# Performance work log

Measured on AMD Instinct MI355X. Metric: run time of the kernel, lower is better.

The kernel has to match this reference:

```python
import jax, jax.numpy as jnp
import numpy as np

B, T, D, KQ, K, V, L = 4, 4096, 256, 32, 4, 8, 4
LN_EPS = 1e-5


def _layernorm(h, g, b):
    mu = h.mean(-1, keepdims=True)
    var = ((h - mu) ** 2).mean(-1, keepdims=True)
    return (h - mu) * jax.lax.rsqrt(var + LN_EPS) * g + b


def _forward(x, attention_mask, Wq, bq, Wk, bk, Wg, bg, W1f, b1f, W2f, b2f,
             ln_g, ln_b, Whh, b_ih, b_hh, Wp, bp, opW1, opb1, opW2, opb2, Wo, bo):
    # ---- DemandRouter ----
    q = x @ Wq + bq                      # [B,T,KQ]
    k = x @ Wk + bk                      # [B,T,KQ]
    sim = jnp.einsum('btk,bsk->bts', q, k) / jnp.sqrt(jnp.float32(KQ))  # [B,T,T]
    mask2 = attention_mask[:, None, :] * attention_mask[:, :, None]
    sim = jnp.where(mask2 == 0, jnp.float32(-1e9), sim)
    gates = jax.nn.sigmoid(x @ Wg + bg)[..., 0]   # [B,T]
    sim = sim * gates[:, :, None]
    _, idx = jax.lax.top_k(sim, K)                # [B,T,K]
    gathered = jax.vmap(lambda xb, ib: xb[ib])(x, idx)  # [B,T,K,D]
    routed_mean = gathered.mean(axis=2)           # [B,T,D]
    # ---- System1Block ----
    ffn = jax.nn.gelu(routed_mean @ W1f + b1f, approximate=False) @ W2f + b2f
    h = _layernorm(routed_mean + ffn, ln_g, ln_b)  # [B,T,D]
    # ---- ProgramGenerator (GRU over zero inputs, h0 = mean-pooled context) ----
    hs = h.mean(axis=1)                           # [B,D]
    outs = []
    for _ in range(L):
        gh = hs @ Whh.T + b_hh                    # [B,3D]
        r = jax.nn.sigmoid(b_ih[:D] + gh[:, :D])
        z = jax.nn.sigmoid(b_ih[D:2 * D] + gh[:, D:2 * D])
        n = jnp.tanh(b_ih[2 * D:] + r * gh[:, 2 * D:])
        hs = (1 - z) * n + z * hs
        outs.append(hs)
    rnn_out = jnp.stack(outs, axis=1)             # [B,L,D]
    program_logits = rnn_out @ Wp + bp            # [B,L,V]
    # ---- NeuralOpLibrary: op outputs are identical across L, so compute once
    # on [B,T,D] and average softmax weights over L (same math as expand+mean).
    op_hidden = jax.nn.relu(jnp.einsum('btd,vde->btve', h, opW1) + opb1)
    op_out = jnp.einsum('btve,ved->btvd', op_hidden, opW2) + opb2  # [B,T,V,D]
    w = jax.nn.softmax(program_logits, axis=-1).mean(axis=1)       # [B,V]
    fused = jnp.einsum('bv,btvd->btd', w, op_out)                   # [B,T,D]
    # ---- pool + output projection ----
    pooled = fused.max(axis=1)                    # [B,D]
    return pooled @ Wo + bo


def setup_inputs() -> dict:
    key = jax.random.key(0)
    ks = jax.random.split(key, 20)
    s = 0.02
    p = lambda i, shape: jax.random.normal(ks[i], shape, jnp.float32) * s
    return {
        'x': jax.random.normal(ks[0], (B, T, D), jnp.float32),
        'attention_mask': jnp.ones((B, T), jnp.float32),
        'Wq': p(1, (D, KQ)), 'bq': jnp.zeros((KQ,), jnp.float32),
        'Wk': p(2, (D, KQ)), 'bk': jnp.zeros((KQ,), jnp.float32),
        'Wg': p(3, (D, 1)), 'bg': jnp.zeros((1,), jnp.float32),
        'W1f': p(4, (D, 2 * D)), 'b1f': jnp.zeros((2 * D,), jnp.float32),
        'W2f': p(5, (2 * D, D)), 'b2f': jnp.zeros((D,), jnp.float32),
        'ln_g': jnp.ones((D,), jnp.float32), 'ln_b': jnp.zeros((D,), jnp.float32),
        'Whh': p(6, (3 * D, D)), 'b_ih': p(7, (3 * D,)), 'b_hh': p(8, (3 * D,)),
        'Wp': p(9, (D, V)), 'bp': jnp.zeros((V,), jnp.float32),
        'opW1': p(10, (V, D, D)), 'opb1': jnp.zeros((V, D), jnp.float32),
        'opW2': p(11, (V, D, D)), 'opb2': jnp.zeros((V, D), jnp.float32),
        'Wo': p(12, (D, D)), 'bo': jnp.zeros((D,), jnp.float32),
    }


def reference(x, attention_mask, Wq, bq, Wk, bk, Wg, bg, W1f, b1f, W2f, b2f,
              ln_g, ln_b, Whh, b_ih, b_hh, Wp, bp, opW1, opb1, opW2, opb2, Wo, bo):
    return _forward(x, attention_mask, Wq, bq, Wk, bk, Wg, bg, W1f, b1f, W2f, b2f,
                    ln_g, ln_b, Whh, b_ih, b_hh, Wp, bp, opW1, opb1, opW2, opb2, Wo, bo)
```

## Files before the change

### kernel.cpp

```cpp
#include <hip/hip_runtime.h>

#define BB 4
#define TT 4096
#define DD 256
#define KQ 32
#define TOPK 4
#define NV 8
#define NL 4
#define MROWS (BB*TT)
#define NSC 8
#define SSPAN 512
#define NCAND (NSC*16)

typedef __attribute__((ext_vector_type(8))) __bf16 bf16x8;
typedef __attribute__((ext_vector_type(4))) float  f32x4;

__device__ __forceinline__ unsigned short f2bf(float f) {
  union { float f; unsigned u; } un; un.f = f;
  unsigned r = un.u + 0x7fffu + ((un.u >> 16) & 1u);
  return (unsigned short)(r >> 16);
}
__device__ __forceinline__ float b2f(unsigned short s) {
  union { unsigned u; float f; } un; un.u = ((unsigned)s) << 16;
  return un.f;
}

__device__ __forceinline__ void ins4(float val, int s, float v[4], int id[4]) {
  if (val <= v[3]) return;
  v[3] = val; id[3] = s;
  #pragma unroll
  for (int j = 3; j > 0; --j) {
    if (v[j] > v[j-1]) {
      float tv = v[j]; v[j] = v[j-1]; v[j-1] = tv;
      int   ti = id[j]; id[j] = id[j-1]; id[j-1] = ti;
    }
  }
}

__global__ __launch_bounds__(256) void prep_weights(
    const float* __restrict__ W1f, const float* __restrict__ W2f,
    const float* __restrict__ opW1, const float* __restrict__ opW2,
    const float* __restrict__ Whh,
    unsigned short* __restrict__ W1ft, unsigned short* __restrict__ W2ft,
    unsigned short* __restrict__ opW1t, unsigned short* __restrict__ opW2t,
    unsigned int* __restrict__ Whhp) {
  int idx = blockIdx.x * 256 + threadIdx.x;
  if (idx < 131072) { int n = idx >> 8, d = idx & 255; W1ft[idx] = f2bf(W1f[d*512 + n]); return; }
  idx -= 131072;
  if (idx < 131072) { int n = idx >> 9, d = idx & 511; W2ft[idx] = f2bf(W2f[d*256 + n]); return; }
  idx -= 131072;
  if (idx < 524288) { int np = idx >> 8, d = idx & 255; int v = np >> 8, e = np & 255;
                      opW1t[idx] = f2bf(opW1[v*65536 + d*256 + e]); return; }
  idx -= 524288;
  if (idx < 524288) { int n = idx >> 11, kp = idx & 2047; int v = kp >> 8, k2 = kp & 255;
                      opW2t[idx] = f2bf(opW2[v*65536 + k2*256 + n]); return; }
  idx -= 524288;
  if (idx < 98304) {
    int dp = idx / 768, j = idx - dp*768;
    unsigned lo = f2bf(Whh[j*256 + 2*dp]);
    unsigned hi = f2bf(Whh[j*256 + 2*dp + 1]);
    Whhp[idx] = lo | (hi << 16);
  }
}

__global__ __launch_bounds__(256) void qk_proj(
    const float* __restrict__ x, const float* __restrict__ Wq, const float* __restrict__ bq,
    const float* __restrict__ Wk, const float* __restrict__ bk,
    float* __restrict__ q, float* __restrict__ kk,
    unsigned short* __restrict__ qbf, unsigned short* __restrict__ kbf) {
  __shared__ float xs[1024];
  int tid = threadIdx.x;
  *(float4*)&xs[tid*4] = *(const float4*)&x[(size_t)blockIdx.x*1024 + tid*4];
  __syncthreads();
  int row = blockIdx.x*4 + (tid >> 6);
  int j = tid & 63;
  int jj = j & 31;
  const float* W = (j < 32) ? Wq : Wk;
  const float* xr = &xs[(tid >> 6) * 256];
  float acc = 0.f;
  #pragma unroll 8
  for (int d = 0; d < 256; ++d) acc += xr[d] * W[d*32 + jj];
  acc += (j < 32) ? bq[jj] : bk[jj];
  float* out = (j < 32) ? q : kk;
  unsigned short* outb = (j < 32) ? qbf : kbf;
  out[(size_t)row*32 + jj] = acc;
  outb[(size_t)row*32 + jj] = f2bf(acc);
}

__global__ __launch_bounds__(256) void sim_scan(
    const unsigned short* __restrict__ qbf, const unsigned short* __restrict__ kbf,
    const float* __restrict__ mask, int* __restrict__ candi, float* __restrict__ candvv) {
  int b = blockIdx.z, sc = blockIdx.y;
  int q0 = blockIdx.x * 64;
  int tid = threadIdx.x;
  int w = tid >> 6, lane = tid & 63;
  int l15 = lane & 15, lhi = lane >> 4;

  __shared__ unsigned short kfr[SSPAN*32];
  __shared__ float ms[SSPAN];
  __shared__ int mflag;

  int qrow = q0 + w*16 + l15;
  bf16x8 qf = *(const bf16x8*)&qbf[((size_t)b*TT + qrow)*32 + lhi*8];
  float mrow = mask[b*TT + qrow];

  float vtop[4]; int itop[4];
  #pragma unroll
  for (int r = 0; r < 4; ++r) { vtop[r] = -__builtin_inff(); itop[r] = 0; }

  int s0 = sc * SSPAN;
  if (tid == 0) mflag = 0;
  __syncthreads();
  int anyzero = 0;
  #pragma unroll
  for (int rr = 0; rr < 2; ++rr) {
    int s = rr*256 + tid;
    const unsigned short* src = &kbf[((size_t)b*TT + s0 + s)*32];
    uint4 d0 = *(const uint4*)(src);
    uint4 d1 = *(const uint4*)(src + 8);
    uint4 d2 = *(const uint4*)(src + 16);
    uint4 d3 = *(const uint4*)(src + 24);
    int fb = (s >> 4)*512 + (s & 15)*8;
    *(uint4*)&kfr[fb +   0] = d0;
    *(uint4*)&kfr[fb + 128] = d1;
    *(uint4*)&kfr[fb + 256] = d2;
    *(uint4*)&kfr[fb + 384] = d3;
    float mv = mask[b*TT + s0 + s];
    ms[s] = mv;
    if (mv == 0.f) anyzero = 1;
  }
  if (anyzero) mflag = 1;
  __syncthreads();
  bool useMask = (mflag != 0) || (mrow == 0.f);
  f32x4 z = {0.f, 0.f, 0.f, 0.f};
  for (int sf = 0; sf < SSPAN/16; sf += 2) {
    bf16x8 a0 = *(const bf16x8*)&kfr[(sf+0)*512 + lane*8];
    bf16x8 a1 = *(const bf16x8*)&kfr[(sf+1)*512 + lane*8];
    f32x4 c0 = __builtin_amdgcn_mfma_f32_16x16x32_bf16(a0, qf, z, 0, 0, 0);
    f32x4 c1 = __builtin_amdgcn_mfma_f32_16x16x32_bf16(a1, qf, z, 0, 0, 0);
    int sb0 = s0 + (sf+0)*16 + lhi*4;
    int sb1 = s0 + (sf+1)*16 + lhi*4;
    #pragma unroll
    for (int r = 0; r < 4; ++r) {
      float v0 = c0[r], v1 = c1[r];
      if (useMask) {
        if (mrow * ms[(sf+0)*16 + lhi*4 + r] == 0.f) v0 = -1e9f;
        if (mrow * ms[(sf+1)*16 + lhi*4 + r] == 0.f) v1 = -1e9f;
      }
      ins4(v0, sb0 + r, vtop, itop);
      ins4(v1, sb1 + r, vtop, itop);
    }
  }
  size_t base = ((size_t)(b*TT + qrow))*NCAND + sc*16 + lhi*4;
  #pragma unroll
  for (int r = 0; r < 4; ++r) { candi[base + r] = itop[r]; candvv[base + r] = vtop[r]; }
}

__global__ __launch_bounds__(256) void refine8(
    const int* __restrict__ candi, const float* __restrict__ candv,
    const float* __restrict__ q, const float* __restrict__ kk,
    const float* __restrict__ mask, int* __restrict__ sel) {
  int tid = threadIdx.x;
  int g = tid >> 5, j = tid & 31;
  int row = blockIdx.x*8 + g;
  int b = row >> 12;
  float v[4]; int id[4];
  const float* cvp = &candv[(size_t)row*NCAND];
  const int*   cip = &candi[(size_t)row*NCAND];
  #pragma unroll
  for (int k2 = 0; k2 < 4; ++k2) { v[k2] = cvp[j + k2*32]; id[k2] = cip[j + k2*32]; }
  int c8[8];
  #pragma unroll
  for (int r = 0; r < 8; ++r) {
    float bv = v[0]; int bi = id[0];
    #pragma unroll
    for (int k2 = 1; k2 < 4; ++k2)
      if (v[k2] > bv || (v[k2] == bv && id[k2] < bi)) { bv = v[k2]; bi = id[k2]; }
    #pragma unroll
    for (int o = 16; o > 0; o >>= 1) {
      float ov = __shfl_xor(bv, o, 32);
      int   oi = __shfl_xor(bi, o, 32);
      if (ov > bv || (ov == bv && oi < bi)) { bv = ov; bi = oi; }
    }
    c8[r] = bi;
    #pragma unroll
    for (int k2 = 0; k2 < 4; ++k2) if (id[k2] == bi) v[k2] = -__builtin_inff();
  }
  int ca = c8[j >> 2];
  int seg = (j & 3) * 8;
  const float* kp = &kk[((size_t)(b << 12) + ca)*32 + seg];
  const float* qp = &q[(size_t)row*32 + seg];
  float pd = 0.f;
  #pragma unroll
  for (int t = 0; t < 8; t += 4) {
    float4 kv = *(const float4*)&kp[t];
    float4 qv = *(const float4*)&qp[t];
    pd += kv.x*qv.x + kv.y*qv.y + kv.z*qv.z + kv.w*qv.w;
  }
  pd += __shfl_xor(pd, 1, 32);
  pd += __shfl_xor(pd, 2, 32);
  if (mask[row] * mask[(b << 12) + ca] == 0.f) pd = -1e9f;
  float dv[8];
  #pragma unroll
  for (int c = 0; c < 8; ++c) dv[c] = __shfl(pd, c*4, 32);
  if (j == 0) {
    int s0 = -1, s1 = -1, s2 = -1, s3 = -1;
    int4 o4;
    #pragma unroll
    for (int r = 0; r < 4; ++r) {
      float bv = -__builtin_inff(); int bi = 0x7fffffff;
      #pragma unroll
      for (int c = 0; c < 8; ++c) {
        int ii = c8[c]; float vv = dv[c];
        if (ii == s0 || ii == s1 || ii == s2 || ii == s3) continue;
        if (vv > bv || (vv == bv && ii < bi)) { bv = vv; bi = ii; }
      }
      if (r == 0) { o4.x = bi; s0 = bi; }
      else if (r == 1) { o4.y = bi; s1 = bi; }
      else if (r == 2) { o4.z = bi; s2 = bi; }
      else { o4.w = bi; s3 = bi; }
    }
    *(int4*)&sel[(size_t)row*4] = o4;
  }
}

__global__ __launch_bounds__(256) void gather_mean(
    const int* __restrict__ sel, const float* __restrict__ x,
    unsigned short* __restrict__ rmb) {
  int tid = threadIdx.x;
  int row = blockIdx.x*4 + (tid >> 6);
  int lane = tid & 63;
  int b = row >> 12;
  int4 s = *(const int4*)&sel[(size_t)row*4];
  const float* xb = &x[(size_t)b*TT*DD];
  float4 a  = *(const float4*)&xb[(size_t)s.x*DD + lane*4];
  float4 bb = *(const float4*)&xb[(size_t)s.y*DD + lane*4];
  float4 cc = *(const float4*)&xb[(size_t)s.z*DD + lane*4];
  float4 e  = *(const float4*)&xb[(size_t)s.w*DD + lane*4];
  ushort4 o;
  o.x = f2bf((a.x + bb.x + cc.x + e.x)*0.25f);
  o.y = f2bf((a.y + bb.y + cc.y + e.y)*0.25f);
  o.z = f2bf((a.z + bb.z + cc.z + e.z)*0.25f);
  o.w = f2bf((a.w + bb.w + cc.w + e.w)*0.25f);
  *(ushort4*)&rmb[(size_t)row*DD + lane*4] = o;
}

template<int EPI>
__global__ __launch_bounds__(256) void gemm_bf16(
    const unsigned short* __restrict__ A, const unsigned short* __restrict__ Bt,
    int Ndim, int Kdim,
    const float* __restrict__ bias,
    const unsigned short* __restrict__ resB,
    const float* __restrict__ auxf,
    float* __restrict__ outF, unsigned short* __restrict__ outB) {
  __shared__ unsigned short As[128*64];
  __shared__ unsigned short Bs[128*64];
  int tid = threadIdx.x;
  int lane = tid & 63, wid = tid >> 6;
  int wm = wid >> 1, wn = wid & 1;
  int l16 = lane & 15, lhi = lane >> 4;
  int m0 = blockIdx.x * 128, n0 = blockIdx.y * 128;
  f32x4 acc[4][4] = {};
  for (int kt = 0; kt < Kdim; kt += 64) {
    __syncthreads();
    #pragma unroll
    for (int i = 0; i < 4; ++i) {
      int L = i*256 + tid;
      int r = L >> 3, c = L & 7;
      int cs = c ^ (r & 7);
      uint4 va = *(const uint4*)(A  + (size_t)(m0 + r)*Kdim + kt + c*8);
      *(uint4*)&As[r*64 + cs*8] = va;
      uint4 vb = *(const uint4*)(Bt + (size_t)(n0 + r)*Kdim + kt + c*8);
      *(uint4*)&Bs[r*64 + cs*8] = vb;
    }
    __syncthreads();
    #pragma unroll
    for (int ks = 0; ks < 2; ++ks) {
      bf16x8 af[4], bfr[4];
      int kc = ks*4 + lhi;
      #pragma unroll
      for (int f = 0; f < 4; ++f) {
        int ra = wm*64 + f*16 + l16;
        af[f]  = *(const bf16x8*)&As[ra*64 + ((kc ^ (ra & 7)))*8];
        int rb = wn*64 + f*16 + l16;
        bfr[f] = *(const bf16x8*)&Bs[rb*64 + ((kc ^ (rb & 7)))*8];
      }
      #pragma unroll
      for (int mf = 0; mf < 4; ++mf)
        #pragma unroll
        for (int nf = 0; nf < 4; ++nf)
          acc[mf][nf] = __builtin_amdgcn_mfma_f32_16x16x32_bf16(af[mf], bfr[nf], acc[mf][nf], 0, 0, 0);
    }
  }
  #pragma unroll
  for (int mf = 0; mf < 4; ++mf) {
    #pragma unroll
    for (int nf = 0; nf < 4; ++nf) {
      #pragma unroll
      for (int r = 0; r < 4; ++r) {
        int row = m0 + wm*64 + mf*16 + lhi*4 + r;
        int col = n0 + wn*64 + nf*16 + l16;
        float v = acc[mf][nf][r];
        if constexpr (EPI == 0) {
          v += bias[col];
          v = 0.5f * v * (1.0f + erff(v * 0.70710678118654752f));
          outB[(size_t)row*Ndim + col] = f2bf(v);
        } else if constexpr (EPI == 1) {
          v += bias[col] + b2f(resB[(size_t)row*Ndim + col]);
          outF[(size_t)row*Ndim + col] = v;
        } else if constexpr (EPI == 2) {
          v += bias[col];
          v = fmaxf(v, 0.0f) * auxf[(row >> 12)*8 + (col >> 8)];
          outB[(size_t)row*Ndim + col] = f2bf(v);
        } else {
          v += auxf[(row >> 12)*256 + col];
          outB[(size_t)row*Ndim + col] = f2bf(v);
        }
      }
    }
  }
}

__global__ __launch_bounds__(256) void gemm64_bf16(
    const unsigned short* __restrict__ A, const unsigned short* __restrict__ Bt,
    int Ndim, int Kdim,
    const float* __restrict__ auxf, unsigned short* __restrict__ outB) {
  __shared__ unsigned short As[64*64];
  __shared__ unsigned short Bs[128*64];
  int tid = threadIdx.x;
  int lane = tid & 63, wn = tid >> 6;
  int l16 = lane & 15, lhi = lane >> 4;
  int m0 = blockIdx.x * 64, n0 = blockIdx.y * 128;
  f32x4 acc[4][2] = {};
  for (int kt = 0; kt < Kdim; kt += 64) {
    __syncthreads();
    #pragma unroll
    for (int i = 0; i < 2; ++i) {
      int L = i*256 + tid;
      int r = L >> 3, c = L & 7;
      int cs = c ^ (r & 7);
      uint4 va = *(const uint4*)(A + (size_t)(m0 + r)*Kdim + kt + c*8);
      *(uint4*)&As[r*64 + cs*8] = va;
    }
    #pragma unroll
    for (int i = 0; i < 4; ++i) {
      int L = i*256 + tid;
      int r = L >> 3, c = L & 7;
      int cs = c ^ (r & 7);
      uint4 vb = *(const uint4*)(Bt + (size_t)(n0 + r)*Kdim + kt + c*8);
      *(uint4*)&Bs[r*64 + cs*8] = vb;
    }
    __syncthreads();
    #pragma unroll
    for (int ks = 0; ks < 2; ++ks) {
      bf16x8 af[4], bfr[2];
      int kc = ks*4 + lhi;
      #pragma unroll
      for (int f = 0; f < 4; ++f) {
        int ra = f*16 + l16;
        af[f] = *(const bf16x8*)&As[ra*64 + ((kc ^ (ra & 7)))*8];
      }
      #pragma unroll
      for (int f = 0; f < 2; ++f) {
        int rb = wn*32 + f*16 + l16;
        bfr[f] = *(const bf16x8*)&Bs[rb*64 + ((kc ^ (rb & 7)))*8];
      }
      #pragma unroll
      for (int mf = 0; mf < 4; ++mf)
        #pragma unroll
        for (int nf = 0; nf < 2; ++nf)
          acc[mf][nf] = __builtin_amdgcn_mfma_f32_16x16x32_bf16(af[mf], bfr[nf], acc[mf][nf], 0, 0, 0);
    }
  }
  #pragma unroll
  for (int mf = 0; mf < 4; ++mf) {
    #pragma unroll
    for (int nf = 0; nf < 2; ++nf) {
      #pragma unroll
      for (int r = 0; r < 4; ++r) {
        int row = m0 + mf*16 + lhi*4 + r;
        int col = n0 + wn*32 + nf*16 + l16;
        float v = acc[mf][nf][r] + auxf[(row >> 12)*256 + col];
        outB[(size_t)row*Ndim + col] = f2bf(v);
      }
    }
  }
}

__global__ __launch_bounds__(256) void ln_kernel(
    const float* __restrict__ preLN, const float* __restrict__ g,
    const float* __restrict__ bta, unsigned short* __restrict__ h) {
  int tid = threadIdx.x;
  int lane = tid & 63;
  int row = blockIdx.x*4 + (tid >> 6);
  float4 v = *(const float4*)&preLN[(size_t)row*256 + lane*4];
  float s = v.x + v.y + v.z + v.w;
  #pragma unroll
  for (int o = 32; o > 0; o >>= 1) s += __shfl_xor(s, o);
  float mu = s * (1.0f/256.0f);
  float4 d; d.x = v.x-mu; d.y = v.y-mu; d.z = v.z-mu; d.w = v.w-mu;
  float s2 = d.x*d.x + d.y*d.y + d.z*d.z + d.w*d.w;
  #pragma unroll
  for (int o = 32; o > 0; o >>= 1) s2 += __shfl_xor(s2, o);
  float rstd = rsqrtf(s2 * (1.0f/256.0f) + 1e-5f);
  float4 gv = *(const float4*)&g[lane*4];
  float4 bv = *(const float4*)&bta[lane*4];
  ushort4 o;
  o.x = f2bf(d.x*rstd*gv.x + bv.x);
  o.y = f2bf(d.y*rstd*gv.y + bv.y);
  o.z = f2bf(d.z*rstd*gv.z + bv.z);
  o.w = f2bf(d.w*rstd*gv.w + bv.w);
  *(ushort4*)&h[(size_t)row*256 + lane*4] = o;
}

__global__ __launch_bounds__(256) void hsum_kernel(const unsigned short* __restrict__ h, float* __restrict__ hpart) {
  int c = blockIdx.x, b = blockIdx.y, d = threadIdx.x;
  const unsigned short* hp = &h[((size_t)(b*TT + c*64))*256 + d];
  float s = 0.f;
  #pragma unroll 8
  for (int i = 0; i < 64; ++i) s += b2f(hp[i*256]);
  hpart[(b*64 + c)*256 + d] = s;
}

__global__ __launch_bounds__(256) void gru_kernel(
    const float* __restrict__ hpart, const unsigned int* __restrict__ Whhp,
    const float* __restrict__ b_ih, const float* __restrict__ b_hh,
    const float* __restrict__ Wp, const float* __restrict__ bp,
    const float* __restrict__ opb2, float* __restrict__ w, float* __restrict__ wb2) {
  int b = blockIdx.x, tid = threadIdx.x;
  __shared__ float hs[256];
  __shared__ float wps[2048];
  __shared__ float lgpart[256];
  __shared__ float lg[8];
  __shared__ float wacc[8];
  float s = 0.f;
  for (int c = 0; c < 64; ++c) s += hpart[(b*64 + c)*256 + tid];
  hs[tid] = s * (1.0f/4096.0f);
  #pragma unroll
  for (int i = 0; i < 8; ++i) wps[i*256 + tid] = Wp[i*256 + tid];
  if (tid < 8) wacc[tid] = 0.f;
  __syncthreads();
  for (int l = 0; l < NL; ++l) {
    float g0 = 0.f, g1 = 0.f, g2 = 0.f;
    #pragma unroll 16
    for (int dp = 0; dp < 128; ++dp) {
      float h0 = hs[2*dp], h1 = hs[2*dp + 1];
      unsigned w0 = Whhp[dp*768 + tid];
      unsigned w1 = Whhp[dp*768 + 256 + tid];
      unsigned w2 = Whhp[dp*768 + 512 + tid];
      g0 += b2f((unsigned short)(w0 & 0xffff))*h0 + b2f((unsigned short)(w0 >> 16))*h1;
      g1 += b2f((unsigned short)(w1 & 0xffff))*h0 + b2f((unsigned short)(w1 >> 16))*h1;
      g2 += b2f((unsigned short)(w2 & 0xffff))*h0 + b2f((unsigned short)(w2 >> 16))*h1;
    }
    g0 += b_hh[tid]; g1 += b_hh[256 + tid]; g2 += b_hh[512 + tid];
    float r = 1.f / (1.f + expf(-(b_ih[tid] + g0)));
    float z = 1.f / (1.f + expf(-(b_ih[256 + tid] + g1)));
    float n = tanhf(b_ih[512 + tid] + r * g2);
    float hnew = (1.f - z) * n + z * hs[tid];
    __syncthreads();
    hs[tid] = hnew;
    __syncthreads();
    {
      int dp2 = tid >> 3;
      float acc = 0.f;
      #pragma unroll
      for (int k2 = 0; k2 < 8; ++k2) acc += hs[dp2 + 32*k2] * wps[tid + 256*k2];
      lgpart[tid] = acc;
    }
    __syncthreads();
    if (tid < 8) {
      float acc = bp[tid];
      #pragma unroll
      for (int j = 0; j < 32; ++j) acc += lgpart[j*8 + tid];
      lg[tid] = acc;
    }
    __syncthreads();
    if (tid == 0) {
      float mx = lg[0];
      #pragma unroll
      for (int i = 1; i < 8; ++i) mx = fmaxf(mx, lg[i]);
      float sm = 0.f; float e[8];
      #pragma unroll
      for (int i = 0; i < 8; ++i) { e[i] = expf(lg[i] - mx); sm += e[i]; }
      #pragma unroll
      for (int i = 0; i < 8; ++i) wacc[i] += e[i] / sm;
    }
    __syncthreads();
  }
  if (tid < 8) w[b*8 + tid] = wacc[tid] * 0.25f;
  float acc = 0.f;
  #pragma unroll
  for (int v = 0; v < 8; ++v) acc += (wacc[v] * 0.25f) * opb2[v*256 + tid];
  wb2[b*256 + tid] = acc;
}

__global__ __launch_bounds__(256) void maxpool_kernel(const unsigned short* __restrict__ fusedB, float* __restrict__ mpart) {
  int c = blockIdx.x, b = blockIdx.y, d = threadIdx.x;
  const unsigned short* fp = &fusedB[((size_t)(b*TT + c*64))*256 + d];
  float m = -__builtin_inff();
  #pragma unroll 8
  for (int i = 0; i < 64; ++i) m = fmaxf(m, b2f(fp[i*256]));
  mpart[(b*64 + c)*256 + d] = m;
}

__global__ __launch_bounds__(256) void outproj_kernel(
    const float* __restrict__ mpart, const float* __restrict__ Wo,
    const float* __restrict__ bo, float* __restrict__ out) {
  int b = blockIdx.x, tid = threadIdx.x;
  __shared__ float pooled[256];
  float m = -__builtin_inff();
  for (int c = 0; c < 64; ++c) m = fmaxf(m, mpart[(b*64 + c)*256 + tid]);
  pooled[tid] = m;
  __syncthreads();
  float acc = bo[tid];
  for (int d = 0; d < 256; ++d) acc += pooled[d] * Wo[d*256 + tid];
  out[b*256 + tid] = acc;
}

extern "C" void kernel_launch(void* const* d_in, const int* in_sizes, int n_in,
                              void* d_out, int out_size, void* d_ws, size_t ws_size,
                              hipStream_t stream) {
  const float* x     = (const float*)d_in[0];
  const float* amask = (const float*)d_in[1];
  const float* Wq    = (const float*)d_in[2];
  const float* bq    = (const float*)d_in[3];
  const float* Wk    = (const float*)d_in[4];
  const float* bk    = (const float*)d_in[5];
  const float* W1f   = (const float*)d_in[8];
  const float* b1f   = (const float*)d_in[9];
  const float* W2f   = (const float*)d_in[10];
  const float* b2f   = (const float*)d_in[11];
  const float* ln_g  = (const float*)d_in[12];
  const float* ln_b  = (const float*)d_in[13];
  const float* Whh   = (const float*)d_in[14];
  const float* b_ih  = (const float*)d_in[15];
  const float* b_hh  = (const float*)d_in[16];
  const float* Wp    = (const float*)d_in[17];
  const float* bp    = (const float*)d_in[18];
  const float* opW1  = (const float*)d_in[19];
  const float* opb1  = (const float*)d_in[20];
  const float* opW2  = (const float*)d_in[21];
  const float* opb2  = (const float*)d_in[22];
  const float* Wo    = (const float*)d_in[23];
  const float* bo    = (const float*)d_in[24];
  (void)in_sizes; (void)n_in; (void)out_size; (void)ws_size;

  char* ws = (char*)d_ws;
  float*          q      = (float*)(ws + 0);
  float*          kk     = (float*)(ws + 2097152);
  unsigned short* qbf    = (unsigned short*)(ws + 4194304);
  unsigned short* kbf    = (unsigned short*)(ws + 5242880);
  int*            candi  = (int*)(ws + 6291456);
  float*          candv  = (float*)(ws + 14680064);
  unsigned short* rmb    = (unsigned short*)(ws + 23068672);
  unsigned short* G1     = (unsigned short*)(ws + 31457280);
  float*          preLN  = (float*)(ws + 48234496);
  unsigned short* G1all  = (unsigned short*)(ws + 0);
  unsigned short* h      = (unsigned short*)(ws + 67108864);
  unsigned short* W1ft   = (unsigned short*)(ws + 75497472);
  unsigned short* W2ft   = (unsigned short*)(ws + 75759616);
  unsigned short* opW1t  = (unsigned short*)(ws + 76021760);
  unsigned short* opW2t  = (unsigned short*)(ws + 77070336);
  unsigned int*   Whhp   = (unsigned int*)(ws + 78118912);
  float*          hpart  = (float*)(ws + 78512128);
  float*          wv     = (float*)(ws + 78774272);
  float*          wb2    = (float*)(ws + 78778368);
  float*          mpart  = (float*)(ws + 78782464);
  unsigned short* fusedB = (unsigned short*)(ws + 79044608);
  int*            sel    = (int*)(ws + 87433216);

  prep_weights<<<5504, 256, 0, stream>>>(W1f, W2f, opW1, opW2, Whh, W1ft, W2ft, opW1t, opW2t, Whhp);
  qk_proj<<<4096, 256, 0, stream>>>(x, Wq, bq, Wk, bk, q, kk, qbf, kbf);
  sim_scan<<<dim3(TT/64, NSC, BB), 256, 0, stream>>>(qbf, kbf, amask, candi, candv);
  refine8<<<MROWS/8, 256, 0, stream>>>(candi, candv, q, kk, amask, sel);
  gather_mean<<<MROWS/4, 256, 0, stream>>>(sel, x, rmb);
  gemm_bf16<0><<<dim3(128, 4), 256, 0, stream>>>(rmb, W1ft, 512, 256, b1f, nullptr, nullptr, nullptr, G1);
  gemm_bf16<1><<<dim3(128, 2), 256, 0, stream>>>(G1, W2ft, 256, 512, b2f, rmb, nullptr, preLN, nullptr);
  ln_kernel<<<4096, 256, 0, stream>>>(preLN, ln_g, ln_b, h);
  hsum_kernel<<<dim3(64, BB), 256, 0, stream>>>(h, hpart);
  gru_kernel<<<4, 256, 0, stream>>>(hpart, Whhp, b_ih, b_hh, Wp, bp, opb2, wv, wb2);
  gemm_bf16<2><<<dim3(128, 16), 256, 0, stream>>>(h, opW1t, 2048, 256, opb1, nullptr, wv, nullptr, G1all);
  gemm64_bf16<<<dim3(256, 2), 256, 0, stream>>>(G1all, opW2t, 256, 2048, wb2, fusedB);
  maxpool_kernel<<<dim3(64, BB), 256, 0, stream>>>(fusedB, mpart);
  outproj_kernel<<<4, 256, 0, stream>>>(mpart, Wo, bo, (float*)d_out);
}
```

Baseline: 301.7 us.

## Stage GEMM bf16 epilogues through LDS and vectorize GRU weight reads

```diff
diff --git a/kernel.cpp b/kernel.cpp
--- a/kernel.cpp
+++ b/kernel.cpp
@@ -43,7 +43,7 @@
     const float* __restrict__ Whh,
     unsigned short* __restrict__ W1ft, unsigned short* __restrict__ W2ft,
     unsigned short* __restrict__ opW1t, unsigned short* __restrict__ opW2t,
-    unsigned int* __restrict__ Whhp) {
+    unsigned int* __restrict__ Whhp2) {
   int idx = blockIdx.x * 256 + threadIdx.x;
   if (idx < 131072) { int n = idx >> 8, d = idx & 255; W1ft[idx] = f2bf(W1f[d*512 + n]); return; }
   idx -= 131072;
@@ -56,10 +56,10 @@
                       opW2t[idx] = f2bf(opW2[v*65536 + k2*256 + n]); return; }
   idx -= 524288;
   if (idx < 98304) {
-    int dp = idx / 768, j = idx - dp*768;
+    int j = idx >> 7, dp = idx & 127;
     unsigned lo = f2bf(Whh[j*256 + 2*dp]);
     unsigned hi = f2bf(Whh[j*256 + 2*dp + 1]);
-    Whhp[idx] = lo | (hi << 16);
+    Whhp2[idx] = lo | (hi << 16);
   }
 }
 
@@ -253,8 +253,9 @@
     const unsigned short* __restrict__ resB,
     const float* __restrict__ auxf,
     float* __restrict__ outF, unsigned short* __restrict__ outB) {
-  __shared__ unsigned short As[128*64];
-  __shared__ unsigned short Bs[128*64];
+  __shared__ unsigned short SMEM[128*132];
+  unsigned short* As = SMEM;
+  unsigned short* Bs = SMEM + 128*64;
   int tid = threadIdx.x;
   int lane = tid & 63, wid = tid >> 6;
   int wm = wid >> 1, wn = wid & 1;
@@ -292,31 +293,49 @@
           acc[mf][nf] = __builtin_amdgcn_mfma_f32_16x16x32_bf16(af[mf], bfr[nf], acc[mf][nf], 0, 0, 0);
     }
   }
-  #pragma unroll
-  for (int mf = 0; mf < 4; ++mf) {
-    #pragma unroll
-    for (int nf = 0; nf < 4; ++nf) {
-      #pragma unroll
-      for (int r = 0; r < 4; ++r) {
-        int row = m0 + wm*64 + mf*16 + lhi*4 + r;
-        int col = n0 + wn*64 + nf*16 + l16;
-        float v = acc[mf][nf][r];
-        if constexpr (EPI == 0) {
-          v += bias[col];
-          v = 0.5f * v * (1.0f + erff(v * 0.70710678118654752f));
-          outB[(size_t)row*Ndim + col] = f2bf(v);
-        } else if constexpr (EPI == 1) {
-          v += bias[col] + b2f(resB[(size_t)row*Ndim + col]);
+  if constexpr (EPI == 1) {
+    #pragma unroll
+    for (int mf = 0; mf < 4; ++mf)
+      #pragma unroll
+      for (int nf = 0; nf < 4; ++nf)
+        #pragma unroll
+        for (int r = 0; r < 4; ++r) {
+          int row = m0 + wm*64 + mf*16 + lhi*4 + r;
+          int col = n0 + wn*64 + nf*16 + l16;
+          float v = acc[mf][nf][r] + bias[col] + b2f(resB[(size_t)row*Ndim + col]);
           outF[(size_t)row*Ndim + col] = v;
-        } else if constexpr (EPI == 2) {
-          v += bias[col];
-          v = fmaxf(v, 0.0f) * auxf[(row >> 12)*8 + (col >> 8)];
-          outB[(size_t)row*Ndim + col] = f2bf(v);
-        } else {
-          v += auxf[(row >> 12)*256 + col];
-          outB[(size_t)row*Ndim + col] = f2bf(v);
         }
-      }
+  } else {
+    __syncthreads();
+    #pragma unroll
+    for (int mf = 0; mf < 4; ++mf) {
+      #pragma unroll
+      for (int nf = 0; nf < 4; ++nf) {
+        #pragma unroll
+        for (int r = 0; r < 4; ++r) {
+          int lrow = wm*64 + mf*16 + lhi*4 + r;
+          int lcol = wn*64 + nf*16 + l16;
+          int row = m0 + lrow, col = n0 + lcol;
+          float v = acc[mf][nf][r];
+          if constexpr (EPI == 0) {
+            v += bias[col];
+            v = 0.5f * v * (1.0f + erff(v * 0.70710678118654752f));
+          } else if constexpr (EPI == 2) {
+            v += bias[col];
+            v = fmaxf(v, 0.0f) * auxf[(row >> 12)*8 + (col >> 8)];
+          } else {
+            v += auxf[(row >> 12)*256 + col];
+          }
+          SMEM[lrow*132 + lcol] = f2bf(v);
+        }
+      }
+    }
+    __syncthreads();
+    #pragma unroll
+    for (int i = 0; i < 8; ++i) {
+      int idx = i*256 + tid;
+      int lrow = idx >> 4, co = (idx & 15)*8;
+      *(uint4*)&outB[(size_t)(m0 + lrow)*Ndim + n0 + co] = *(const uint4*)&SMEM[lrow*132 + co];
     }
   }
 }
@@ -325,8 +344,9 @@
     const unsigned short* __restrict__ A, const unsigned short* __restrict__ Bt,
     int Ndim, int Kdim,
     const float* __restrict__ auxf, unsigned short* __restrict__ outB) {
-  __shared__ unsigned short As[64*64];
-  __shared__ unsigned short Bs[128*64];
+  __shared__ unsigned short SMEM[64*192 + 64];
+  unsigned short* As = SMEM;
+  unsigned short* Bs = SMEM + 64*64;
   int tid = threadIdx.x;
   int lane = tid & 63, wn = tid >> 6;
   int l16 = lane & 15, lhi = lane >> 4;
@@ -372,18 +392,26 @@
           acc[mf][nf] = __builtin_amdgcn_mfma_f32_16x16x32_bf16(af[mf], bfr[nf], acc[mf][nf], 0, 0, 0);
     }
   }
+  __syncthreads();
   #pragma unroll
   for (int mf = 0; mf < 4; ++mf) {
     #pragma unroll
     for (int nf = 0; nf < 2; ++nf) {
       #pragma unroll
       for (int r = 0; r < 4; ++r) {
-        int row = m0 + mf*16 + lhi*4 + r;
-        int col = n0 + wn*32 + nf*16 + l16;
-        float v = acc[mf][nf][r] + auxf[(row >> 12)*256 + col];
-        outB[(size_t)row*Ndim + col] = f2bf(v);
-      }
-    }
+        int lrow = mf*16 + lhi*4 + r;
+        int lcol = wn*32 + nf*16 + l16;
+        float v = acc[mf][nf][r] + auxf[((m0 + lrow) >> 12)*256 + n0 + lcol];
+        SMEM[lrow*132 + lcol] = f2bf(v);
+      }
+    }
+  }
+  __syncthreads();
+  #pragma unroll
+  for (int i = 0; i < 4; ++i) {
+    int idx = i*256 + tid;
+    int lrow = idx >> 4, co = (idx & 15)*8;
+    *(uint4*)&outB[(size_t)(m0 + lrow)*Ndim + n0 + co] = *(const uint4*)&SMEM[lrow*132 + co];
   }
 }
 
@@ -423,7 +451,7 @@
 }
 
 __global__ __launch_bounds__(256) void gru_kernel(
-    const float* __restrict__ hpart, const unsigned int* __restrict__ Whhp,
+    const float* __restrict__ hpart, const unsigned int* __restrict__ Whhp2,
     const float* __restrict__ b_ih, const float* __restrict__ b_hh,
     const float* __restrict__ Wp, const float* __restrict__ bp,
     const float* __restrict__ opb2, float* __restrict__ w, float* __restrict__ wb2) {
@@ -434,6 +462,7 @@
   __shared__ float lg[8];
   __shared__ float wacc[8];
   float s = 0.f;
+  #pragma unroll
   for (int c = 0; c < 64; ++c) s += hpart[(b*64 + c)*256 + tid];
   hs[tid] = s * (1.0f/4096.0f);
   #pragma unroll
@@ -441,18 +470,26 @@
   if (tid < 8) wacc[tid] = 0.f;
   __syncthreads();
   for (int l = 0; l < NL; ++l) {
-    float g0 = 0.f, g1 = 0.f, g2 = 0.f;
-    #pragma unroll 16
-    for (int dp = 0; dp < 128; ++dp) {
-      float h0 = hs[2*dp], h1 = hs[2*dp + 1];
-      unsigned w0 = Whhp[dp*768 + tid];
-      unsigned w1 = Whhp[dp*768 + 256 + tid];
-      unsigned w2 = Whhp[dp*768 + 512 + tid];
-      g0 += b2f((unsigned short)(w0 & 0xffff))*h0 + b2f((unsigned short)(w0 >> 16))*h1;
-      g1 += b2f((unsigned short)(w1 & 0xffff))*h0 + b2f((unsigned short)(w1 >> 16))*h1;
-      g2 += b2f((unsigned short)(w2 & 0xffff))*h0 + b2f((unsigned short)(w2 >> 16))*h1;
-    }
-    g0 += b_hh[tid]; g1 += b_hh[256 + tid]; g2 += b_hh[512 + tid];
+    float gg[3];
+    #pragma unroll
+    for (int p = 0; p < 3; ++p) {
+      int j = p*256 + tid;
+      const uint4* wp4 = (const uint4*)&Whhp2[(size_t)j*128];
+      float acc = 0.f;
+      #pragma unroll 8
+      for (int i = 0; i < 32; ++i) {
+        uint4 w4 = wp4[i];
+        const float* hb = &hs[i*8];
+        acc += b2f((unsigned short)(w4.x & 0xffff))*hb[0] + b2f((unsigned short)(w4.x >> 16))*hb[1];
+        acc += b2f((unsigned short)(w4.y & 0xffff))*hb[2] + b2f((unsigned short)(w4.y >> 16))*hb[3];
+        acc += b2f((unsigned short)(w4.z & 0xffff))*hb[4] + b2f((unsigned short)(w4.z >> 16))*hb[5];
+        acc += b2f((unsigned short)(w4.w & 0xffff))*hb[6] + b2f((unsigned short)(w4.w >> 16))*hb[7];
+      }
+      gg[p] = acc;
+    }
+    float g0 = gg[0] + b_hh[tid];
+    float g1 = gg[1] + b_hh[256 + tid];
+    float g2 = gg[2] + b_hh[512 + tid];
     float r = 1.f / (1.f + expf(-(b_ih[tid] + g0)));
     float z = 1.f / (1.f + expf(-(b_ih[256 + tid] + g1)));
     float n = tanhf(b_ih[512 + tid] + r * g2);
@@ -561,7 +598,7 @@
   unsigned short* W2ft   = (unsigned short*)(ws + 75759616);
   unsigned short* opW1t  = (unsigned short*)(ws + 76021760);
   unsigned short* opW2t  = (unsigned short*)(ws + 77070336);
-  unsigned int*   Whhp   = (unsigned int*)(ws + 78118912);
+  unsigned int*   Whhp2  = (unsigned int*)(ws + 78118912);
   float*          hpart  = (float*)(ws + 78512128);
   float*          wv     = (float*)(ws + 78774272);
   float*          wb2    = (float*)(ws + 78778368);
@@ -569,7 +606,7 @@
   unsigned short* fusedB = (unsigned short*)(ws + 79044608);
   int*            sel    = (int*)(ws + 87433216);
 
-  prep_weights<<<5504, 256, 0, stream>>>(W1f, W2f, opW1, opW2, Whh, W1ft, W2ft, opW1t, opW2t, Whhp);
+  prep_weights<<<5504, 256, 0, stream>>>(W1f, W2f, opW1, opW2, Whh, W1ft, W2ft, opW1t, opW2t, Whhp2);
   qk_proj<<<4096, 256, 0, stream>>>(x, Wq, bq, Wk, bk, q, kk, qbf, kbf);
   sim_scan<<<dim3(TT/64, NSC, BB), 256, 0, stream>>>(qbf, kbf, amask, candi, candv);
   refine8<<<MROWS/8, 256, 0, stream>>>(candi, candv, q, kk, amask, sel);
@@ -578,7 +615,7 @@
   gemm_bf16<1><<<dim3(128, 2), 256, 0, stream>>>(G1, W2ft, 256, 512, b2f, rmb, nullptr, preLN, nullptr);
   ln_kernel<<<4096, 256, 0, stream>>>(preLN, ln_g, ln_b, h);
   hsum_kernel<<<dim3(64, BB), 256, 0, stream>>>(h, hpart);
-  gru_kernel<<<4, 256, 0, stream>>>(hpart, Whhp, b_ih, b_hh, Wp, bp, opb2, wv, wb2);
+  gru_kernel<<<4, 256, 0, stream>>>(hpart, Whhp2, b_ih, b_hh, Wp, bp, opb2, wv, wb2);
   gemm_bf16<2><<<dim3(128, 16), 256, 0, stream>>>(h, opW1t, 2048, 256, opb1, nullptr, wv, nullptr, G1all);
   gemm64_bf16<<<dim3(256, 2), 256, 0, stream>>>(G1all, opW2t, 256, 2048, wb2, fusedB);
   maxpool_kernel<<<dim3(64, BB), 256, 0, stream>>>(fusedB, mpart);
```

New measurement: 335.1 us. 1.11x slower.
